# Optimization experiments

Measured on AMD Instinct MI355X. Metric: run time of the kernel, lower is better.

## Reference

```python
import jax, jax.numpy as jnp
import numpy as np

N_NODES = 20000
N_EDGES = 320000
N_GRAPHS = 512
VOCAB = 32
D = 256
K_HOPS = 4
EPS = 1e-5


def setup_inputs() -> dict:
    key = jax.random.key(0)
    ks = jax.random.split(key, 16)
    s = 0.02
    return {
        "x": jax.random.randint(ks[0], (N_NODES,), 0, VOCAB),
        "edge_index": jax.random.randint(ks[1], (2, N_EDGES), 0, N_NODES),
        "batch": jnp.sort(jax.random.randint(ks[2], (N_NODES,), 0, N_GRAPHS)),
        "node_table": jax.random.normal(ks[3], (VOCAB, D)) * s,
        "sg_W": jax.random.normal(ks[4], (D, D)) * s,
        "sg_b": jnp.zeros((D,)),
        "W1": jax.random.normal(ks[5], (D, 2 * D)) * s,
        "b1": jnp.zeros((2 * D,)),
        "g1": jnp.ones((2 * D,)),
        "be1": jnp.zeros((2 * D,)),
        "W2": jax.random.normal(ks[6], (2 * D, D)) * s,
        "b2": jnp.zeros((D,)),
        "g2": jnp.ones((D,)),
        "be2": jnp.zeros((D,)),
        "W3": jax.random.normal(ks[7], (D, 1)) * s,
        "b3": jnp.zeros((1,)),
    }


def _batchnorm(z, g, b):
    # BatchNorm1d in training-mode math (batch statistics), deterministic.
    m = z.mean(axis=0)
    v = z.var(axis=0)
    return (z - m) * jax.lax.rsqrt(v + EPS) * g + b


def reference(x, edge_index, batch, node_table, sg_W, sg_b,
              W1, b1, g1, be1, W2, b2, g2, be2, W3, b3):
    n = node_table.shape[0] and x.shape[0]  # N nodes
    h = node_table[x]  # [N, D] node embedding lookup (NodeEncoder)

    # SGConv: add self-loops, symmetric normalization, K hops, then Linear.
    loop = jnp.arange(n, dtype=edge_index.dtype)
    src = jnp.concatenate([edge_index[0], loop])
    dst = jnp.concatenate([edge_index[1], loop])
    deg = jax.ops.segment_sum(jnp.ones_like(dst, dtype=h.dtype), dst, num_segments=n)
    dinv = jnp.where(deg > 0, jax.lax.rsqrt(jnp.maximum(deg, 1.0)), 0.0)
    norm = (dinv[src] * dinv[dst])[:, None]  # [E+N, 1]
    for _ in range(K_HOPS):
        h = jax.ops.segment_sum(h[src] * norm, dst, num_segments=n)
    h = h @ sg_W + sg_b  # [N, D]

    # global_add_pool over graphs (dropout = identity in eval)
    hg = jax.ops.segment_sum(h, batch, num_segments=N_GRAPHS)  # [G, D]

    hg = jax.nn.relu(_batchnorm(hg @ W1 + b1, g1, be1))  # [G, 2D]
    hg = jax.nn.relu(_batchnorm(hg @ W2 + b2, g2, be2))  # [G, D]
    return hg @ W3 + b3  # [G, num_tasks]
```

## Files before the change

kernel.cpp:

```cpp
#include <hip/hip_runtime.h>

#define N_NODES  20000
#define N_EDGES  320000
#define N_GRAPHS 512
#define VOCAB    32
#define D        256
#define TWO_D    512
#define EPS      1e-5f
#define CAP      64
#define HB       (N_NODES / 16)


__device__ __forceinline__ unsigned int pack_bf2(float a, float b) {
    unsigned int ua = __float_as_uint(a);
    unsigned int ub = __float_as_uint(b);
    ua = (ua + 0x7FFFu + ((ua >> 16) & 1u)) >> 16;
    ub = (ub + 0x7FFFu + ((ub >> 16) & 1u)) >> 16;
    return ua | (ub << 16);
}
__device__ __forceinline__ float bf_lo(unsigned int v) { return __uint_as_float(v << 16); }
__device__ __forceinline__ float bf_hi(unsigned int v) { return __uint_as_float(v & 0xFFFF0000u); }


__global__ __launch_bounds__(512) void zero_fold_kernel(const int* __restrict__ batch,
                                                        int* __restrict__ cnt,
                                                        float* __restrict__ cs1,
                                                        float* __restrict__ cs2,
                                                        float* __restrict__ S,
                                                        int* __restrict__ gstart,
                                                        const float* __restrict__ table,
                                                        const float* __restrict__ sgW,
                                                        const float* __restrict__ sg_b,
                                                        const float* __restrict__ W1,
                                                        float* __restrict__ G,
                                                        float* __restrict__ u) {
    __shared__ float trow[D];
    __shared__ float frow[D];
    int bid = blockIdx.x, tid = threadIdx.x;
    if (bid < 40) {
        int i = bid * 512 + tid;
        if (i < N_NODES) {
            cnt[i] = 0;
            int b = batch[i];
            if (i == 0) { for (int g = 0; g <= b; ++g) gstart[g] = 0; }
            else { int pb = batch[i - 1]; for (int g = pb + 1; g <= b; ++g) gstart[g] = i; }
            if (i == N_NODES - 1) { for (int g = b + 1; g <= N_GRAPHS; ++g) gstart[g] = N_NODES; }
        }
        if (i < 2 * TWO_D) cs1[i] = 0.f;
        if (i < 2 * D) cs2[i] = 0.f;
        if (i < N_GRAPHS * VOCAB) S[i] = 0.f;
    } else {
        int r = bid - 40;
        if (r < VOCAB) {
            if (tid < D) trow[tid] = table[r * D + tid];
            __syncthreads();
            if (tid < D) {
                float acc = 0.f;
                for (int k = 0; k < D; ++k) acc += trow[k] * sgW[k * D + tid];
                frow[tid] = acc;
            }
        } else {
            if (tid < D) frow[tid] = sg_b[tid];
        }
        __syncthreads();
        float acc = 0.f;
        for (int k = 0; k < D; ++k) acc += frow[k] * W1[k * TWO_D + tid];
        float* dst = (r < VOCAB) ? (G + r * TWO_D) : u;
        dst[tid] = acc;
    }
}


__global__ __launch_bounds__(256) void bucket_kernel(const int* __restrict__ src,
                                                     const int* __restrict__ dst,
                                                     int* __restrict__ cnt,
                                                     int* __restrict__ buckets) {
    int e = blockIdx.x * 256 + threadIdx.x;
    if (e >= N_EDGES) return;
    int d = dst[e];
    int slot = atomicAdd(&cnt[d], 1);
    if (slot < CAP) buckets[d * CAP + slot] = src[e];
}


__global__ __launch_bounds__(256) void hop1_kernel(const int* __restrict__ x,
                                                   const int* __restrict__ cnt,
                                                   const int* __restrict__ buckets,
                                                   unsigned int* __restrict__ rout) {
    int node = (blockIdx.x << 4) | (threadIdx.x >> 4);
    int sub = threadIdx.x & 15;
    int qbase = (threadIdx.x & 63) & 48;
    int f0 = sub * 2, f1 = f0 + 1;
    int cd = cnt[node];
    float dn = rsqrtf((float)(cd + 1));
    int xf = x[node];
    float ax = (xf == f0) ? dn : 0.f;
    float ay = (xf == f1) ? dn : 0.f;
    float bx = 0.f, by = 0.f;
    int n = min(cd, CAP);
    const int* bk = buckets + node * CAP;
    for (int w = 0; w < n; w += 16) {
        int lw = min(16, n - w);
        int bkv = bk[w + sub];
        int j = 0;
        for (; j + 2 <= lw; j += 2) {
            int s0 = __shfl(bkv, qbase + j);
            int s1 = __shfl(bkv, qbase + j + 1);
            int x0 = x[s0], x1 = x[s1];
            float d0 = rsqrtf((float)(cnt[s0] + 1));
            float d1 = rsqrtf((float)(cnt[s1] + 1));
            ax += (x0 == f0) ? d0 : 0.f;
            ay += (x0 == f1) ? d0 : 0.f;
            bx += (x1 == f0) ? d1 : 0.f;
            by += (x1 == f1) ? d1 : 0.f;
        }
        if (j < lw) {
            int s0 = __shfl(bkv, qbase + j);
            int x0 = x[s0];
            float d0 = rsqrtf((float)(cnt[s0] + 1));
            ax += (x0 == f0) ? d0 : 0.f;
            ay += (x0 == f1) ? d0 : 0.f;
        }
    }
    float q = 1.f / (float)(cd + 1);
    rout[node * 16 + sub] = pack_bf2(q * (ax + bx), q * (ay + by));
}


__global__ __launch_bounds__(256) void hop_kernel(const unsigned int* __restrict__ rin,
                                                  unsigned int* __restrict__ rout,
                                                  const int* __restrict__ cnt,
                                                  const int* __restrict__ buckets) {
    int node = (blockIdx.x << 4) | (threadIdx.x >> 4);
    int sub = threadIdx.x & 15;
    int qbase = (threadIdx.x & 63) & 48;
    int cd = cnt[node];
    unsigned int self = rin[node * 16 + sub];
    float ax = bf_lo(self), ay = bf_hi(self);
    float bx = 0.f, by = 0.f, cx = 0.f, cy = 0.f, dx = 0.f, dy = 0.f;
    int n = min(cd, CAP);
    const int* bk = buckets + node * CAP;
    for (int w = 0; w < n; w += 16) {
        int lw = min(16, n - w);
        int bkv = bk[w + sub];
        int j = 0;
        for (; j + 4 <= lw; j += 4) {
            int s0 = __shfl(bkv, qbase + j);
            int s1 = __shfl(bkv, qbase + j + 1);
            int s2 = __shfl(bkv, qbase + j + 2);
            int s3 = __shfl(bkv, qbase + j + 3);
            unsigned int v0 = rin[s0 * 16 + sub], v1 = rin[s1 * 16 + sub];
            unsigned int v2 = rin[s2 * 16 + sub], v3 = rin[s3 * 16 + sub];
            ax += bf_lo(v0); ay += bf_hi(v0);
            bx += bf_lo(v1); by += bf_hi(v1);
            cx += bf_lo(v2); cy += bf_hi(v2);
            dx += bf_lo(v3); dy += bf_hi(v3);
        }
        for (; j < lw; ++j) {
            int s = __shfl(bkv, qbase + j);
            unsigned int v = rin[s * 16 + sub];
            ax += bf_lo(v); ay += bf_hi(v);
        }
    }
    float q = 1.f / (float)(cd + 1);
    rout[node * 16 + sub] = pack_bf2(q * (ax + bx + cx + dx), q * (ay + by + cy + dy));
}


__global__ __launch_bounds__(256) void hop4s_kernel(const unsigned int* __restrict__ rin,
                                                    const int* __restrict__ cnt,
                                                    const int* __restrict__ buckets,
                                                    const int* __restrict__ batch,
                                                    float* __restrict__ S) {
    int node = (blockIdx.x << 4) | (threadIdx.x >> 4);
    int sub = threadIdx.x & 15;
    int qbase = (threadIdx.x & 63) & 48;
    int cd = cnt[node];
    unsigned int self = rin[node * 16 + sub];
    float ax = bf_lo(self), ay = bf_hi(self);
    float bx = 0.f, by = 0.f, cx = 0.f, cy = 0.f, dx = 0.f, dy = 0.f;
    int n = min(cd, CAP);
    const int* bk = buckets + node * CAP;
    for (int w = 0; w < n; w += 16) {
        int lw = min(16, n - w);
        int bkv = bk[w + sub];
        int j = 0;
        for (; j + 4 <= lw; j += 4) {
            int s0 = __shfl(bkv, qbase + j);
            int s1 = __shfl(bkv, qbase + j + 1);
            int s2 = __shfl(bkv, qbase + j + 2);
            int s3 = __shfl(bkv, qbase + j + 3);
            unsigned int v0 = rin[s0 * 16 + sub], v1 = rin[s1 * 16 + sub];
            unsigned int v2 = rin[s2 * 16 + sub], v3 = rin[s3 * 16 + sub];
            ax += bf_lo(v0); ay += bf_hi(v0);
            bx += bf_lo(v1); by += bf_hi(v1);
            cx += bf_lo(v2); cy += bf_hi(v2);
            dx += bf_lo(v3); dy += bf_hi(v3);
        }
        for (; j < lw; ++j) {
            int s = __shfl(bkv, qbase + j);
            unsigned int v = rin[s * 16 + sub];
            ax += bf_lo(v); ay += bf_hi(v);
        }
    }
    float dinv = rsqrtf((float)(cd + 1));
    int g = batch[node];
    atomicAdd(&S[g * VOCAB + sub * 2],     dinv * (ax + bx + cx + dx));
    atomicAdd(&S[g * VOCAB + sub * 2 + 1], dinv * (ay + by + cy + dy));
}


__global__ __launch_bounds__(256) void lin1_kernel(const float* __restrict__ S_,
                                                   const int* __restrict__ gstart,
                                                   const float* __restrict__ G,
                                                   const float* __restrict__ u,
                                                   const float* __restrict__ b1,
                                                   float* __restrict__ z1,
                                                   float* __restrict__ cs1) {
    __shared__ float S[8 * VOCAB];
    int g0 = blockIdx.x * 8;
    int tid = threadIdx.x;
    S[tid] = S_[g0 * VOCAB + tid];
    __syncthreads();
    float a0[8], a1[8];
#pragma unroll
    for (int i = 0; i < 8; ++i) { a0[i] = 0.f; a1[i] = 0.f; }
    for (int k = 0; k < VOCAB; ++k) {
        float w0 = G[k * TWO_D + tid];
        float w1 = G[k * TWO_D + tid + 256];
#pragma unroll
        for (int i = 0; i < 8; ++i) {
            float r = S[i * VOCAB + k];
            a0[i] += r * w0; a1[i] += r * w1;
        }
    }
    float u0 = u[tid], u1 = u[tid + 256];
    float c0 = b1[tid], c1 = b1[tid + 256];
    float s0 = 0.f, ss0 = 0.f, s1 = 0.f, ss1 = 0.f;
#pragma unroll
    for (int i = 0; i < 8; ++i) {
        float gc = (float)(gstart[g0 + i + 1] - gstart[g0 + i]);
        float z0v = a0[i] + gc * u0 + c0;
        float z1v = a1[i] + gc * u1 + c1;
        z1[(g0 + i) * TWO_D + tid]       = z0v;
        z1[(g0 + i) * TWO_D + tid + 256] = z1v;
        s0 += z0v; ss0 += z0v * z0v;
        s1 += z1v; ss1 += z1v * z1v;
    }
    atomicAdd(&cs1[tid], s0);
    atomicAdd(&cs1[TWO_D + tid], ss0);
    atomicAdd(&cs1[tid + 256], s1);
    atomicAdd(&cs1[TWO_D + tid + 256], ss1);
}


__global__ __launch_bounds__(256) void lin2_kernel(const float* __restrict__ z1,
                                                   const float* __restrict__ cs1,
                                                   const float* __restrict__ g1,
                                                   const float* __restrict__ be1,
                                                   const float* __restrict__ W2,
                                                   const float* __restrict__ b2,
                                                   float* __restrict__ z2,
                                                   float* __restrict__ cs2) {
    __shared__ float A[TWO_D], C[TWO_D];
    __shared__ float rows[4 * TWO_D];
    int tid = threadIdx.x;
    int g0 = blockIdx.x * 4;
    for (int k = tid; k < TWO_D; k += 256) {
        float m = cs1[k] * (1.f / N_GRAPHS);
        float var = cs1[TWO_D + k] * (1.f / N_GRAPHS) - m * m;
        float a = rsqrtf(var + EPS) * g1[k];
        A[k] = a;
        C[k] = be1[k] - m * a;
    }
    __syncthreads();
    for (int idx = tid; idx < 4 * TWO_D; idx += 256) {
        int k = idx & (TWO_D - 1);
        float v = z1[g0 * TWO_D + idx] * A[k] + C[k];
        rows[idx] = v > 0.f ? v : 0.f;
    }
    __syncthreads();
    float acc[4] = {0.f, 0.f, 0.f, 0.f};
    for (int k = 0; k < TWO_D; ++k) {
        float wv = W2[k * D + tid];
        acc[0] += rows[k] * wv;
        acc[1] += rows[TWO_D + k] * wv;
        acc[2] += rows[2 * TWO_D + k] * wv;
        acc[3] += rows[3 * TWO_D + k] * wv;
    }
    float bb = b2[tid];
    float s = 0.f, ss = 0.f;
#pragma unroll
    for (int i = 0; i < 4; ++i) {
        float zv = acc[i] + bb;
        z2[(g0 + i) * D + tid] = zv;
        s += zv; ss += zv * zv;
    }
    atomicAdd(&cs2[tid], s);
    atomicAdd(&cs2[D + tid], ss);
}


__global__ __launch_bounds__(64) void head_kernel(const float* __restrict__ z2,
                                                  const float* __restrict__ cs2,
                                                  const float* __restrict__ g2,
                                                  const float* __restrict__ be2,
                                                  const float* __restrict__ W3,
                                                  const float* __restrict__ b3,
                                                  float* __restrict__ out) {
    __shared__ float A[D], C[D];
    int g = blockIdx.x;
    int lane = threadIdx.x;
    for (int k = lane; k < D; k += 64) {
        float m = cs2[k] * (1.f / N_GRAPHS);
        float var = cs2[D + k] * (1.f / N_GRAPHS) - m * m;
        float a = rsqrtf(var + EPS) * g2[k];
        A[k] = a;
        C[k] = be2[k] - m * a;
    }
    __syncthreads();
    float acc = 0.f;
    for (int k = lane; k < D; k += 64) {
        float v = z2[g * D + k] * A[k] + C[k];
        v = v > 0.f ? v : 0.f;
        acc += v * W3[k];
    }
    for (int off = 32; off; off >>= 1) acc += __shfl_down(acc, off);
    if (lane == 0) out[g] = acc + b3[0];
}


extern "C" void kernel_launch(void* const* d_in, const int* in_sizes, int n_in,
                              void* d_out, int out_size, void* d_ws, size_t ws_size,
                              hipStream_t stream) {
    const int*   x     = (const int*)d_in[0];
    const int*   e_src = (const int*)d_in[1];
    const int*   e_dst = (const int*)d_in[1] + N_EDGES;
    const int*   batch = (const int*)d_in[2];
    const float* table = (const float*)d_in[3];
    const float* sg_W  = (const float*)d_in[4];
    const float* sg_b  = (const float*)d_in[5];
    const float* W1    = (const float*)d_in[6];
    const float* b1    = (const float*)d_in[7];
    const float* g1    = (const float*)d_in[8];
    const float* be1   = (const float*)d_in[9];
    const float* W2    = (const float*)d_in[10];
    const float* b2    = (const float*)d_in[11];
    const float* g2    = (const float*)d_in[12];
    const float* be2   = (const float*)d_in[13];
    const float* W3    = (const float*)d_in[14];
    const float* b3    = (const float*)d_in[15];
    float*       out   = (float*)d_out;

    char* p = (char*)d_ws;
    auto alloc = [&](size_t bytes) { char* q = p; p += (bytes + 15) & ~size_t(15); return q; };
    unsigned int* m_a = (unsigned int*)alloc((size_t)N_NODES * 16 * 4);
    unsigned int* m_b = (unsigned int*)alloc((size_t)N_NODES * 16 * 4);
    int*   cnt     = (int*)  alloc((size_t)N_NODES * 4);
    int*   buckets = (int*)  alloc((size_t)N_NODES * CAP * 4);
    int*   gstart  = (int*)  alloc((size_t)(N_GRAPHS + 1) * 4);
    float* S       = (float*)alloc((size_t)N_GRAPHS * VOCAB * 4);
    float* G       = (float*)alloc((size_t)VOCAB * TWO_D * 4);
    float* u       = (float*)alloc((size_t)TWO_D * 4);
    float* z1      = (float*)alloc((size_t)N_GRAPHS * TWO_D * 4);
    float* z2      = (float*)alloc((size_t)N_GRAPHS * D * 4);
    float* cs1     = (float*)alloc((size_t)2 * TWO_D * 4);
    float* cs2     = (float*)alloc((size_t)2 * D * 4);

    zero_fold_kernel<<<73, 512, 0, stream>>>(batch, cnt, cs1, cs2, S, gstart,
                                             table, sg_W, sg_b, W1, G, u);
    bucket_kernel<<<(N_EDGES + 255) / 256, 256, 0, stream>>>(e_src, e_dst, cnt, buckets);

    hop1_kernel <<<HB, 256, 0, stream>>>(x, cnt, buckets, m_b);
    hop_kernel  <<<HB, 256, 0, stream>>>(m_b, m_a, cnt, buckets);
    hop_kernel  <<<HB, 256, 0, stream>>>(m_a, m_b, cnt, buckets);
    hop4s_kernel<<<HB, 256, 0, stream>>>(m_b, cnt, buckets, batch, S);

    lin1_kernel<<<N_GRAPHS / 8, 256, 0, stream>>>(S, gstart, G, u, b1, z1, cs1);
    lin2_kernel<<<N_GRAPHS / 4, 256, 0, stream>>>(z1, cs1, g1, be1, W2, b2, z2, cs2);
    head_kernel<<<N_GRAPHS, 64, 0, stream>>>(z2, cs2, g2, be2, W3, b3, out);
}
```

Baseline: 116.9 us.

## Store edge buckets as 16-bit indices and fold weight precompute into bucket kernel

Adjacency buckets now hold source indices as unsigned 16-bit values instead of 32-bit ints, halving bucket storage and read traffic. Each lane loads two packed indices per 32-bit word, and the hop kernels walk 32 neighbours per load window. The table·sgW·W1 fold now runs in extra blocks of the bucket-building kernel rather than in the zeroing kernel, so it overlaps with the atomic bucketing. This relies on node count fitting in 16 bits (20000 < 65536), and the packed layout adds some shift and mask work per neighbour.

```diff
diff --git a/kernel.cpp b/kernel.cpp
--- a/kernel.cpp
+++ b/kernel.cpp
@@ -22,70 +22,72 @@
 __device__ __forceinline__ float bf_hi(unsigned int v) { return __uint_as_float(v & 0xFFFF0000u); }
 
 
-__global__ __launch_bounds__(512) void zero_fold_kernel(const int* __restrict__ batch,
-                                                        int* __restrict__ cnt,
-                                                        float* __restrict__ cs1,
-                                                        float* __restrict__ cs2,
-                                                        float* __restrict__ S,
-                                                        int* __restrict__ gstart,
-                                                        const float* __restrict__ table,
-                                                        const float* __restrict__ sgW,
-                                                        const float* __restrict__ sg_b,
-                                                        const float* __restrict__ W1,
-                                                        float* __restrict__ G,
-                                                        float* __restrict__ u) {
+__global__ __launch_bounds__(512) void zero_kernel(const int* __restrict__ batch,
+                                                   int* __restrict__ cnt,
+                                                   float* __restrict__ cs1,
+                                                   float* __restrict__ cs2,
+                                                   float* __restrict__ S,
+                                                   int* __restrict__ gstart) {
+    int i = blockIdx.x * 512 + threadIdx.x;
+    if (i < N_NODES) {
+        cnt[i] = 0;
+        int b = batch[i];
+        if (i == 0) { for (int g = 0; g <= b; ++g) gstart[g] = 0; }
+        else { int pb = batch[i - 1]; for (int g = pb + 1; g <= b; ++g) gstart[g] = i; }
+        if (i == N_NODES - 1) { for (int g = b + 1; g <= N_GRAPHS; ++g) gstart[g] = N_NODES; }
+    }
+    if (i < 2 * TWO_D) cs1[i] = 0.f;
+    if (i < 2 * D) cs2[i] = 0.f;
+    if (i < N_GRAPHS * VOCAB) S[i] = 0.f;
+}
+
+
+__global__ __launch_bounds__(256) void bucket_fold_kernel(const int* __restrict__ src,
+                                                          const int* __restrict__ dst,
+                                                          int* __restrict__ cnt,
+                                                          unsigned short* __restrict__ bk16,
+                                                          const float* __restrict__ table,
+                                                          const float* __restrict__ sgW,
+                                                          const float* __restrict__ sg_b,
+                                                          const float* __restrict__ W1,
+                                                          float* __restrict__ G,
+                                                          float* __restrict__ u) {
     __shared__ float trow[D];
     __shared__ float frow[D];
     int bid = blockIdx.x, tid = threadIdx.x;
-    if (bid < 40) {
-        int i = bid * 512 + tid;
-        if (i < N_NODES) {
-            cnt[i] = 0;
-            int b = batch[i];
-            if (i == 0) { for (int g = 0; g <= b; ++g) gstart[g] = 0; }
-            else { int pb = batch[i - 1]; for (int g = pb + 1; g <= b; ++g) gstart[g] = i; }
-            if (i == N_NODES - 1) { for (int g = b + 1; g <= N_GRAPHS; ++g) gstart[g] = N_NODES; }
-        }
-        if (i < 2 * TWO_D) cs1[i] = 0.f;
-        if (i < 2 * D) cs2[i] = 0.f;
-        if (i < N_GRAPHS * VOCAB) S[i] = 0.f;
+    if (bid < 1250) {
+        int e = bid * 256 + tid;
+        int d = dst[e];
+        int slot = atomicAdd(&cnt[d], 1);
+        if (slot < CAP) bk16[d * CAP + slot] = (unsigned short)src[e];
     } else {
-        int r = bid - 40;
+        int r = bid - 1250;
         if (r < VOCAB) {
-            if (tid < D) trow[tid] = table[r * D + tid];
+            trow[tid] = table[r * D + tid];
             __syncthreads();
-            if (tid < D) {
-                float acc = 0.f;
-                for (int k = 0; k < D; ++k) acc += trow[k] * sgW[k * D + tid];
-                frow[tid] = acc;
-            }
+            float acc = 0.f;
+            for (int k = 0; k < D; ++k) acc += trow[k] * sgW[k * D + tid];
+            frow[tid] = acc;
         } else {
-            if (tid < D) frow[tid] = sg_b[tid];
+            frow[tid] = sg_b[tid];
         }
         __syncthreads();
-        float acc = 0.f;
-        for (int k = 0; k < D; ++k) acc += frow[k] * W1[k * TWO_D + tid];
-        float* dst = (r < VOCAB) ? (G + r * TWO_D) : u;
-        dst[tid] = acc;
-    }
-}
-
-
-__global__ __launch_bounds__(256) void bucket_kernel(const int* __restrict__ src,
-                                                     const int* __restrict__ dst,
-                                                     int* __restrict__ cnt,
-                                                     int* __restrict__ buckets) {
-    int e = blockIdx.x * 256 + threadIdx.x;
-    if (e >= N_EDGES) return;
-    int d = dst[e];
-    int slot = atomicAdd(&cnt[d], 1);
-    if (slot < CAP) buckets[d * CAP + slot] = src[e];
+        float a0 = 0.f, a1 = 0.f;
+        for (int k = 0; k < D; ++k) {
+            float rv = frow[k];
+            a0 += rv * W1[k * TWO_D + tid];
+            a1 += rv * W1[k * TWO_D + tid + 256];
+        }
+        float* dstp = (r < VOCAB) ? (G + r * TWO_D) : u;
+        dstp[tid] = a0;
+        dstp[tid + 256] = a1;
+    }
 }
 
 
 __global__ __launch_bounds__(256) void hop1_kernel(const int* __restrict__ x,
                                                    const int* __restrict__ cnt,
-                                                   const int* __restrict__ buckets,
+                                                   const unsigned short* __restrict__ bk16,
                                                    unsigned int* __restrict__ rout) {
     int node = (blockIdx.x << 4) | (threadIdx.x >> 4);
     int sub = threadIdx.x & 15;
@@ -98,14 +100,14 @@
     float ay = (xf == f1) ? dn : 0.f;
     float bx = 0.f, by = 0.f;
     int n = min(cd, CAP);
-    const int* bk = buckets + node * CAP;
-    for (int w = 0; w < n; w += 16) {
-        int lw = min(16, n - w);
-        int bkv = bk[w + sub];
+    const unsigned int* row = (const unsigned int*)(bk16 + node * CAP);
+    for (int w = 0; w < n; w += 32) {
+        int lw = min(32, n - w);
+        unsigned int bkv = row[(w >> 1) + sub];
         int j = 0;
         for (; j + 2 <= lw; j += 2) {
-            int s0 = __shfl(bkv, qbase + j);
-            int s1 = __shfl(bkv, qbase + j + 1);
+            unsigned int pp = __shfl(bkv, qbase + (j >> 1));
+            int s0 = pp & 0xFFFF, s1 = pp >> 16;
             int x0 = x[s0], x1 = x[s1];
             float d0 = rsqrtf((float)(cnt[s0] + 1));
             float d1 = rsqrtf((float)(cnt[s1] + 1));
@@ -115,7 +117,8 @@
             by += (x1 == f1) ? d1 : 0.f;
         }
         if (j < lw) {
-            int s0 = __shfl(bkv, qbase + j);
+            unsigned int pp = __shfl(bkv, qbase + (j >> 1));
+            int s0 = pp & 0xFFFF;
             int x0 = x[s0];
             float d0 = rsqrtf((float)(cnt[s0] + 1));
             ax += (x0 == f0) ? d0 : 0.f;
@@ -130,7 +133,7 @@
 __global__ __launch_bounds__(256) void hop_kernel(const unsigned int* __restrict__ rin,
                                                   unsigned int* __restrict__ rout,
                                                   const int* __restrict__ cnt,
-                                                  const int* __restrict__ buckets) {
+                                                  const unsigned short* __restrict__ bk16) {
     int node = (blockIdx.x << 4) | (threadIdx.x >> 4);
     int sub = threadIdx.x & 15;
     int qbase = (threadIdx.x & 63) & 48;
@@ -139,16 +142,16 @@
     float ax = bf_lo(self), ay = bf_hi(self);
     float bx = 0.f, by = 0.f, cx = 0.f, cy = 0.f, dx = 0.f, dy = 0.f;
     int n = min(cd, CAP);
-    const int* bk = buckets + node * CAP;
-    for (int w = 0; w < n; w += 16) {
-        int lw = min(16, n - w);
-        int bkv = bk[w + sub];
+    const unsigned int* row = (const unsigned int*)(bk16 + node * CAP);
+    for (int w = 0; w < n; w += 32) {
+        int lw = min(32, n - w);
+        unsigned int bkv = row[(w >> 1) + sub];
         int j = 0;
         for (; j + 4 <= lw; j += 4) {
-            int s0 = __shfl(bkv, qbase + j);
-            int s1 = __shfl(bkv, qbase + j + 1);
-            int s2 = __shfl(bkv, qbase + j + 2);
-            int s3 = __shfl(bkv, qbase + j + 3);
+            unsigned int pp0 = __shfl(bkv, qbase + (j >> 1));
+            unsigned int pp1 = __shfl(bkv, qbase + (j >> 1) + 1);
+            int s0 = pp0 & 0xFFFF, s1 = pp0 >> 16;
+            int s2 = pp1 & 0xFFFF, s3 = pp1 >> 16;
             unsigned int v0 = rin[s0 * 16 + sub], v1 = rin[s1 * 16 + sub];
             unsigned int v2 = rin[s2 * 16 + sub], v3 = rin[s3 * 16 + sub];
             ax += bf_lo(v0); ay += bf_hi(v0);
@@ -157,7 +160,8 @@
             dx += bf_lo(v3); dy += bf_hi(v3);
         }
         for (; j < lw; ++j) {
-            int s = __shfl(bkv, qbase + j);
+            unsigned int pp = __shfl(bkv, qbase + (j >> 1));
+            int s = (j & 1) ? (int)(pp >> 16) : (int)(pp & 0xFFFF);
             unsigned int v = rin[s * 16 + sub];
             ax += bf_lo(v); ay += bf_hi(v);
         }
@@ -169,7 +173,7 @@
 
 __global__ __launch_bounds__(256) void hop4s_kernel(const unsigned int* __restrict__ rin,
                                                     const int* __restrict__ cnt,
-                                                    const int* __restrict__ buckets,
+                                                    const unsigned short* __restrict__ bk16,
                                                     const int* __restrict__ batch,
                                                     float* __restrict__ S) {
     int node = (blockIdx.x << 4) | (threadIdx.x >> 4);
@@ -180,16 +184,16 @@
     float ax = bf_lo(self), ay = bf_hi(self);
     float bx = 0.f, by = 0.f, cx = 0.f, cy = 0.f, dx = 0.f, dy = 0.f;
     int n = min(cd, CAP);
-    const int* bk = buckets + node * CAP;
-    for (int w = 0; w < n; w += 16) {
-        int lw = min(16, n - w);
-        int bkv = bk[w + sub];
+    const unsigned int* row = (const unsigned int*)(bk16 + node * CAP);
+    for (int w = 0; w < n; w += 32) {
+        int lw = min(32, n - w);
+        unsigned int bkv = row[(w >> 1) + sub];
         int j = 0;
         for (; j + 4 <= lw; j += 4) {
-            int s0 = __shfl(bkv, qbase + j);
-            int s1 = __shfl(bkv, qbase + j + 1);
-            int s2 = __shfl(bkv, qbase + j + 2);
-            int s3 = __shfl(bkv, qbase + j + 3);
+            unsigned int pp0 = __shfl(bkv, qbase + (j >> 1));
+            unsigned int pp1 = __shfl(bkv, qbase + (j >> 1) + 1);
+            int s0 = pp0 & 0xFFFF, s1 = pp0 >> 16;
+            int s2 = pp1 & 0xFFFF, s3 = pp1 >> 16;
             unsigned int v0 = rin[s0 * 16 + sub], v1 = rin[s1 * 16 + sub];
             unsigned int v2 = rin[s2 * 16 + sub], v3 = rin[s3 * 16 + sub];
             ax += bf_lo(v0); ay += bf_hi(v0);
@@ -198,7 +202,8 @@
             dx += bf_lo(v3); dy += bf_hi(v3);
         }
         for (; j < lw; ++j) {
-            int s = __shfl(bkv, qbase + j);
+            unsigned int pp = __shfl(bkv, qbase + (j >> 1));
+            int s = (j & 1) ? (int)(pp >> 16) : (int)(pp & 0xFFFF);
             unsigned int v = rin[s * 16 + sub];
             ax += bf_lo(v); ay += bf_hi(v);
         }
@@ -354,10 +359,10 @@
 
     char* p = (char*)d_ws;
     auto alloc = [&](size_t bytes) { char* q = p; p += (bytes + 15) & ~size_t(15); return q; };
-    unsigned int* m_a = (unsigned int*)alloc((size_t)N_NODES * 16 * 4);
-    unsigned int* m_b = (unsigned int*)alloc((size_t)N_NODES * 16 * 4);
-    int*   cnt     = (int*)  alloc((size_t)N_NODES * 4);
-    int*   buckets = (int*)  alloc((size_t)N_NODES * CAP * 4);
+    unsigned int*   m_a  = (unsigned int*)alloc((size_t)N_NODES * 16 * 4);
+    unsigned int*   m_b  = (unsigned int*)alloc((size_t)N_NODES * 16 * 4);
+    int*            cnt  = (int*)alloc((size_t)N_NODES * 4);
+    unsigned short* bk16 = (unsigned short*)alloc((size_t)N_NODES * CAP * 2);
     int*   gstart  = (int*)  alloc((size_t)(N_GRAPHS + 1) * 4);
     float* S       = (float*)alloc((size_t)N_GRAPHS * VOCAB * 4);
     float* G       = (float*)alloc((size_t)VOCAB * TWO_D * 4);
@@ -367,14 +372,14 @@
     float* cs1     = (float*)alloc((size_t)2 * TWO_D * 4);
     float* cs2     = (float*)alloc((size_t)2 * D * 4);
 
-    zero_fold_kernel<<<73, 512, 0, stream>>>(batch, cnt, cs1, cs2, S, gstart,
-                                             table, sg_W, sg_b, W1, G, u);
-    bucket_kernel<<<(N_EDGES + 255) / 256, 256, 0, stream>>>(e_src, e_dst, cnt, buckets);
-
-    hop1_kernel <<<HB, 256, 0, stream>>>(x, cnt, buckets, m_b);
-    hop_kernel  <<<HB, 256, 0, stream>>>(m_b, m_a, cnt, buckets);
-    hop_kernel  <<<HB, 256, 0, stream>>>(m_a, m_b, cnt, buckets);
-    hop4s_kernel<<<HB, 256, 0, stream>>>(m_b, cnt, buckets, batch, S);
+    zero_kernel<<<40, 512, 0, stream>>>(batch, cnt, cs1, cs2, S, gstart);
+    bucket_fold_kernel<<<1283, 256, 0, stream>>>(e_src, e_dst, cnt, bk16,
+                                                 table, sg_W, sg_b, W1, G, u);
+
+    hop1_kernel <<<HB, 256, 0, stream>>>(x, cnt, bk16, m_b);
+    hop_kernel  <<<HB, 256, 0, stream>>>(m_b, m_a, cnt, bk16);
+    hop_kernel  <<<HB, 256, 0, stream>>>(m_a, m_b, cnt, bk16);
+    hop4s_kernel<<<HB, 256, 0, stream>>>(m_b, cnt, bk16, batch, S);
 
     lin1_kernel<<<N_GRAPHS / 8, 256, 0, stream>>>(S, gstart, G, u, b1, z1, cs1);
     lin2_kernel<<<N_GRAPHS / 4, 256, 0, stream>>>(z1, cs1, g1, be1, W2, b2, z2, cs2);
```

New measurement: 124.9 us. +6.9%, slower.
